# Kernel tuning notes

Measured on AMD Instinct MI355X. Metric: run time of the kernel, lower is better.

The kernel has to match this reference:

```python
import jax, jax.numpy as jnp
import numpy as np


def conv2d(x, w, pad=0, groups=1, bias=None):
    out = jax.lax.conv_general_dilated(
        x, w, (1, 1), [(pad, pad), (pad, pad)],
        dimension_numbers=('NCHW', 'OIHW', 'NCHW'), feature_group_count=groups)
    return out if bias is None else out + bias[None, :, None, None]


def l2norm(t):
    # F.normalize(t, dim=-1): divide by max(||t||_2, 1e-12)
    return t / jnp.maximum(jnp.sqrt(jnp.sum(t * t, axis=-1, keepdims=True)), 1e-12)


def chan_attn(q, k, v, temp, heads):
    # transposed (channel) attention: contract over N=H*W, softmax over small channel dim
    b, _, h, w = v.shape
    n = h * w
    q = l2norm(q.reshape(b, heads, -1, n))
    k = l2norm(k.reshape(b, heads, -1, n))
    v = v.reshape(b, heads, -1, n)
    attn = jax.nn.softmax(jnp.einsum('bhdn,bhen->bhde', q, k) * temp, axis=-1)
    return jnp.einsum('bhde,bhen->bhdn', attn, v).reshape(b, -1, h, w)


def nearest_resize(x, H, W):
    # torch F.interpolate(mode='nearest'): idx = floor(i * in/out)
    hi, wi = x.shape[2], x.shape[3]
    iy = jnp.arange(H) * hi // H
    ix = jnp.arange(W) * wi // W
    return x[:, :, iy][:, :, :, ix]


def deform_conv(x, offsets, w, bias, k, pad, groups):
    # torchvision DeformConv2d, stride=1, dilation=1, offset layout [B, 2*k*k, H, W] as (dy, dx) pairs
    B, Cin, H, W = x.shape
    K2 = k * k
    off = offsets.reshape(B, K2, 2, H, W)
    ky, kx = jnp.meshgrid(jnp.arange(k), jnp.arange(k), indexing='ij')
    py = (jnp.arange(H)[None, None, :, None] - pad) + ky.reshape(1, K2, 1, 1) + off[:, :, 0]
    px = (jnp.arange(W)[None, None, None, :] - pad) + kx.reshape(1, K2, 1, 1) + off[:, :, 1]
    y0f = jnp.floor(py); x0f = jnp.floor(px)
    wy = (py - y0f)[:, None]  # [B,1,K2,H,W]
    wx = (px - x0f)[:, None]
    y0 = y0f.astype(jnp.int32); x0 = x0f.astype(jnp.int32)
    xf = x.reshape(B, Cin, H * W)

    def gather(yi, xi):
        valid = ((yi >= 0) & (yi < H) & (xi >= 0) & (xi < W)).astype(x.dtype)
        idx = (jnp.clip(yi, 0, H - 1) * W + jnp.clip(xi, 0, W - 1)).reshape(B, 1, -1)
        v = jnp.take_along_axis(xf, idx, axis=2).reshape(B, Cin, K2, H, W)
        return v * valid[:, None]

    s = (gather(y0, x0) * (1 - wy) * (1 - wx)
         + gather(y0, x0 + 1) * (1 - wy) * wx
         + gather(y0 + 1, x0) * wy * (1 - wx)
         + gather(y0 + 1, x0 + 1) * wy * wx)  # [B, Cin, K2, H, W]
    g = groups
    s = s.reshape(B, g, Cin // g, K2, H, W)
    wg = w.reshape(g, w.shape[0] // g, Cin // g, K2)
    out = jnp.einsum('bgckhw,gock->bgohw', s, wg).reshape(B, -1, H, W)
    return out + bias[None, :, None, None]


def scconv(x, w_k2, w_k3, w_k4):
    B, C, H, W = x.shape
    p = x.reshape(B, C, H // 2, 2, W // 2, 2).mean(axis=(3, 5))  # AvgPool2d(2,2)
    a = jax.nn.sigmoid(nearest_resize(conv2d(p, w_k2, pad=0), H, W))
    return conv2d(conv2d(x, w_k3, pad=1) * a, w_k4, pad=1)


def layernorm_c(x, g, b):
    # LayerNorm over channel dim of NCHW (applied as [B, HW, C] in the original)
    b_, c, h, w = x.shape
    t = x.reshape(b_, c, h * w).transpose(0, 2, 1)
    mu = t.mean(-1, keepdims=True)
    var = ((t - mu) ** 2).mean(-1, keepdims=True)
    t = (t - mu) / jnp.sqrt(var + 1e-5) * g + b
    return t.transpose(0, 2, 1).reshape(b_, c, h, w)


def _forward(x, y, temp, w_po, w_lp1, w_lp2, ln_g, ln_b, temp_in, w_qkv, w_qkvd,
             w_mproj, w_c3, w_k2, w_k3, w_k4, w_d3, b_d3, w_d5, b_d5, w_d7, b_d7,
             w_pw, b_pw):
    b, c, h, w = x.shape
    heads = 8
    # --- Multi_Receptive_Attentive_Prompts ---
    l1 = conv2d(x, w_lp1)
    l2 = conv2d(x, w_lp2, pad=1)
    xn = layernorm_c(x, ln_g, ln_b)
    qkv = conv2d(conv2d(xn, w_qkv), w_qkvd, pad=1, groups=c)
    qi, ki, vi = jnp.split(qkv, 3, axis=1)
    xg = x + conv2d(chan_attn(qi, ki, vi, temp_in, heads), w_mproj)
    prompt = conv2d(jnp.concatenate([l1, l2, xg], axis=1), w_c3, pad=1)
    # --- Temporal_Alignment ---
    offs = scconv(jnp.concatenate([x, y], axis=1), w_k2, w_k3, w_k4)  # [B,166,H,W]
    f3 = jax.nn.relu(deform_conv(x, offs[:, :18], w_d3, b_d3, 3, 1, 8))
    f5 = jax.nn.relu(deform_conv(x, offs[:, 18:68], w_d5, b_d5, 5, 2, 8))
    f7 = jax.nn.relu(deform_conv(x, offs[:, 68:166], w_d7, b_d7, 7, 3, 8))
    k_feat = conv2d(jnp.concatenate([f3, f5, f7], axis=1), w_pw, bias=b_pw)
    # --- prompted channel attention ---
    q_feat = jnp.concatenate([x, prompt], axis=1)  # 2c channels -> d_q = 2c/heads
    out = chan_attn(q_feat, k_feat, x, temp, heads)  # [B, 2c, H, W]
    return conv2d(out, w_po)


def setup_inputs() -> dict:
    key = jax.random.key(0)
    ks = jax.random.split(key, 16)
    C, B, H, W = 32, 2, 128, 128
    r = lambda k, shp: jax.random.normal(k, shp, dtype=jnp.float32) * 0.05
    return {
        'x': jax.random.normal(ks[0], (B, C, H, W), dtype=jnp.float32),
        'y': jax.random.normal(ks[1], (B, C, H, W), dtype=jnp.float32),
        'temp': jnp.ones((1, 8, 1, 1), jnp.float32),
        'w_po': r(ks[2], (C, 2 * C, 1, 1)),
        'w_lp1': r(ks[3], (C, C, 1, 1)),
        'w_lp2': r(ks[4], (C, C, 3, 3)),
        'ln_g': jnp.ones((C,), jnp.float32),
        'ln_b': jnp.zeros((C,), jnp.float32),
        'temp_in': jnp.ones((1, 8, 1, 1), jnp.float32),
        'w_qkv': r(ks[5], (3 * C, C, 1, 1)),
        'w_qkvd': r(ks[6], (3 * C, 3, 3, 3)),  # groups=C: in/groups = 3
        'w_mproj': r(ks[7], (C, C, 1, 1)),
        'w_c3': r(ks[8], (C, 3 * C, 3, 3)),
        'w_k2': r(ks[9], (166, 2 * C, 3, 3)),
        'w_k3': r(ks[10], (166, 2 * C, 3, 3)),
        'w_k4': r(ks[11], (166, 166, 3, 3)),
        'w_d3': r(ks[12], (C, C // 8, 3, 3)),
        'b_d3': jnp.zeros((C,), jnp.float32),
        'w_d5': r(ks[13], (C, C // 8, 5, 5)),
        'b_d5': jnp.zeros((C,), jnp.float32),
        'w_d7': r(ks[14], (C, C // 8, 7, 7)),
        'b_d7': jnp.zeros((C,), jnp.float32),
        'w_pw': r(ks[15], (C, 3 * C, 1, 1)),
        'b_pw': jnp.zeros((C,), jnp.float32),
    }


def reference(x, y, temp, w_po, w_lp1, w_lp2, ln_g, ln_b, temp_in, w_qkv, w_qkvd,
              w_mproj, w_c3, w_k2, w_k3, w_k4, w_d3, b_d3, w_d5, b_d5, w_d7, b_d7,
              w_pw, b_pw):
    return _forward(x, y, temp, w_po, w_lp1, w_lp2, ln_g, ln_b, temp_in, w_qkv,
                    w_qkvd, w_mproj, w_c3, w_k2, w_k3, w_k4, w_d3, b_d3, w_d5,
                    b_d5, w_d7, b_d7, w_pw, b_pw)
```

## Files before the change

### kernel.cpp

```cpp
#include <hip/hip_runtime.h>
#include <hip/hip_bf16.h>
#include <hip/hip_fp16.h>


constexpr int B = 2, C = 32, H = 128, W = 128, N = H * W;

using bh8   = __attribute__((ext_vector_type(8))) short;
using f32x4 = __attribute__((ext_vector_type(4))) float;

__device__ __forceinline__ ushort f2bf(float v) {
  __hip_bfloat16 h = __float2bfloat16(v);
  return *(ushort*)&h;
}
__device__ __forceinline__ float bf2f(ushort u) {
  union { unsigned int i; float f; } w; w.i = ((unsigned int)u) << 16; return w.f;
}

__global__ __launch_bounds__(256) void k_prep(const float* __restrict__ x,
                                              const float* __restrict__ y,
                                              const float* __restrict__ ln_g,
                                              const float* __restrict__ ln_b,
                                              float* __restrict__ cat2,
                                              ushort* __restrict__ xtb,
                                              ushort* __restrict__ cat2b,
                                              ushort* __restrict__ xnb,
                                              ushort* __restrict__ poolb) {
  __shared__ float tile[C][257];
  const int b = blockIdx.y, n0 = blockIdx.x * 256, tid = threadIdx.x;
  const int n = n0 + tid;
  const int prow = blockIdx.x;
  for (int c = 0; c < C; c++) {
    float v = x[(size_t)(b * C + c) * N + n];
    tile[c][tid] = v;
    cat2[(size_t)(b * 64 + c) * N + n] = v;
  }
  __syncthreads();
  {
    float s = 0.f, ss = 0.f;
#pragma unroll
    for (int c = 0; c < C; c++) { const float v = tile[c][tid]; s += v; ss += v * v; }
    const float mu = s * (1.f / C);
    const float var = ss * (1.f / C) - mu * mu;
    const float inv = rsqrtf(var + 1e-5f);
    ushort xo[32];
#pragma unroll
    for (int c = 0; c < C; c++)
      xo[c] = f2bf((tile[c][tid] - mu) * inv * ln_g[c] + ln_b[c]);
    ushort* dp = xnb + ((size_t)b * N + n) * 32;
#pragma unroll
    for (int k = 0; k < 4; k++) *(bh8*)(dp + k * 8) = *(const bh8*)&xo[k * 8];
  }
  for (int i = tid; i < C * 256; i += 256) {
    int c = i & 31, nl = i >> 5;
    const ushort bv = f2bf(tile[c][nl]);
    xtb[((size_t)b * N + n0 + nl) * 32 + c] = bv;
    cat2b[((size_t)b * N + n0 + nl) * 64 + c] = bv;
  }
  for (int i = tid; i < 2048; i += 256) {
    const int ox = i >> 5, c = i & 31;
    const float pv = 0.25f * (tile[c][2 * ox] + tile[c][2 * ox + 1]
                            + tile[c][128 + 2 * ox] + tile[c][128 + 2 * ox + 1]);
    poolb[((size_t)b * 4096 + prow * 64 + ox) * 64 + c] = f2bf(pv);
  }
  __syncthreads();
  for (int c = 0; c < C; c++) {
    float v = y[(size_t)(b * C + c) * N + n];
    tile[c][tid] = v;
    cat2[(size_t)(b * 64 + 32 + c) * N + n] = v;
  }
  __syncthreads();
  for (int i = tid; i < C * 256; i += 256) {
    int c = i & 31, nl = i >> 5;
    cat2b[((size_t)b * N + n0 + nl) * 64 + 32 + c] = f2bf(tile[c][nl]);
  }
  for (int i = tid; i < 2048; i += 256) {
    const int ox = i >> 5, c = i & 31;
    const float pv = 0.25f * (tile[c][2 * ox] + tile[c][2 * ox + 1]
                            + tile[c][128 + 2 * ox] + tile[c][128 + 2 * ox + 1]);
    poolb[((size_t)b * 4096 + prow * 64 + ox) * 64 + 32 + c] = f2bf(pv);
  }
}

struct WEnt { const float* src; ushort* dst; int cout_real, cin_real, kc32, total; };
struct WArgs { WEnt e[5]; };

__global__ __launch_bounds__(256) void k_wpack(WArgs a) {
  const WEnt en = a.e[blockIdx.y];
  const int tk = 9 * en.kc32;
  for (int i = blockIdx.x * 256 + threadIdx.x; i < en.total; i += gridDim.x * 256) {
    const int co = i / tk, rem = i - co * tk;
    const int t = rem / en.kc32, ci = rem - t * en.kc32;
    float v = 0.f;
    if (co < en.cout_real && ci < en.cin_real)
      v = en.src[((size_t)co * en.cin_real + ci) * 9 + t];
    en.dst[i] = f2bf(v);
  }
}

__global__ __launch_bounds__(256)
void k_castw(const float* __restrict__ a, ushort* __restrict__ da, int na,
             const float* __restrict__ b2, ushort* __restrict__ db, int nb2) {
  const int i = blockIdx.x * 256 + threadIdx.x;
  if (i < na) da[i] = f2bf(a[i]);
  if (i < nb2) db[i] = f2bf(b2[i]);
}

template <int MT, int KC>
__global__ __launch_bounds__(256)
void k_gemm1x1(const ushort* __restrict__ in, int in_cs,
               const ushort* __restrict__ wq, const float* __restrict__ bias,
               float* __restrict__ out, long out_bs) {
  const int tid = threadIdx.x, b = blockIdx.y;
  const int px0 = blockIdx.x * 64 + (tid >> 6) * 16;
  const int lane = tid & 63, q = lane >> 4, n = lane & 15, q8 = q * 8;
  f32x4 acc[MT];
#pragma unroll
  for (int mt = 0; mt < MT; mt++) acc[mt] = (f32x4){0.f, 0.f, 0.f, 0.f};
  const ushort* ib = in + (size_t)b * N * in_cs;
#pragma unroll
  for (int kc = 0; kc < KC; kc++) {
    const bh8 bb = *(const bh8*)(ib + (size_t)(px0 + n) * in_cs + kc * 32 + q8);
#pragma unroll
    for (int mt = 0; mt < MT; mt++) {
      const bh8 a = *(const bh8*)(wq + (size_t)(mt * 16 + n) * (KC * 32) + kc * 32 + q8);
      acc[mt] = __builtin_amdgcn_mfma_f32_16x16x32_bf16(a, bb, acc[mt], 0, 0, 0);
    }
  }
  float* ob = out + (size_t)b * out_bs;
#pragma unroll
  for (int mt = 0; mt < MT; mt++)
#pragma unroll
    for (int r = 0; r < 4; r++) {
      const int co = mt * 16 + q * 4 + r;
      const float bv = bias ? bias[co] : 0.f;
      ob[(size_t)co * N + px0 + n] = acc[mt][r] + bv;
    }
}

__global__ __launch_bounds__(256)
void k_conv3m(const ushort* __restrict__ xin, long in_bs, int in_cs, int ih, int iw,
              const ushort* __restrict__ wp, int kchunks, int cout_real,
              void* __restrict__ outp, long out_bs, int out_coff,
              int oh, int ow, int pad, int omode, int out_cs, int store_tot,
              const float* __restrict__ gatep) {
  __shared__ ushort smem[17408];
  ushort* xt = smem;
  const int tid = threadIdx.x, b = blockIdx.z;
  const int y0 = blockIdx.x * 2, co0 = blockIdx.y * 32;
  const int wv = tid >> 6, lane = tid & 63;
  const int row_sel = wv >> 1, col0 = (wv & 1) * 64;
  const int q = lane >> 4, n = lane & 15, q8 = q * 8;
  const int kc32 = kchunks * 32;
  const ushort* xb = xin + (size_t)b * in_bs;

  f32x4 acc[2][4];
#pragma unroll
  for (int mt = 0; mt < 2; mt++)
#pragma unroll
    for (int nb = 0; nb < 4; nb++) acc[mt][nb] = (f32x4){0.f, 0.f, 0.f, 0.f};

  for (int cc = 0; cc < kchunks; cc++) {
    __syncthreads();
    for (int i = tid; i < 2080; i += 256) {
      const int qq = i & 3, rc = i >> 2;
      const int r = rc / 130, c = rc - r * 130;
      const int yy = y0 - pad + r, xx = c - pad;
      bh8 v = {0, 0, 0, 0, 0, 0, 0, 0};
      if (yy >= 0 && yy < ih && xx >= 0 && xx < iw)
        v = *(const bh8*)(xb + ((size_t)yy * iw + xx) * in_cs + cc * 32 + qq * 8);
      *(bh8*)&xt[rc * 32 + qq * 8] = v;
    }
    __syncthreads();
#pragma unroll
    for (int t = 0; t < 9; t++) {
      const int dy = t / 3, dx = t - dy * 3;
      bh8 a[2], bb[4];
#pragma unroll
      for (int mt = 0; mt < 2; mt++)
        a[mt] = *(const bh8*)(wp + (size_t)((co0 + mt * 16 + n) * 9 + t) * kc32 + cc * 32 + q8);
#pragma unroll
      for (int nb = 0; nb < 4; nb++)
        bb[nb] = *(const bh8*)&xt[((row_sel + dy) * 130 + col0 + nb * 16 + n + dx) * 32 + q8];
#pragma unroll
      for (int mt = 0; mt < 2; mt++)
#pragma unroll
        for (int nb = 0; nb < 4; nb++)
          acc[mt][nb] = __builtin_amdgcn_mfma_f32_16x16x32_bf16(a[mt], bb[nb], acc[mt][nb], 0, 0, 0);
    }
  }

  const size_t osp = (size_t)oh * ow;
  if (omode == 0) {
    const int oy = y0 + row_sel;
    float* ob = (float*)outp + (size_t)b * out_bs + (size_t)out_coff * osp + (size_t)oy * ow;
#pragma unroll
    for (int mt = 0; mt < 2; mt++)
#pragma unroll
      for (int r = 0; r < 4; r++) {
        const int co = co0 + mt * 16 + q * 4 + r;
        if (co < cout_real) {
#pragma unroll
          for (int nb = 0; nb < 4; nb++) {
            const int px = col0 + nb * 16 + n;
            if (px < ow) ob[(size_t)co * osp + px] = acc[mt][nb][r];
          }
        }
      }
  } else if (omode == 1) {
    __syncthreads();
#pragma unroll
    for (int mt = 0; mt < 2; mt++)
#pragma unroll
      for (int nb = 0; nb < 4; nb++) {
        const int px = col0 + nb * 16 + n;
        ushort4 o;
        o.x = f2bf(acc[mt][nb][0]); o.y = f2bf(acc[mt][nb][1]);
        o.z = f2bf(acc[mt][nb][2]); o.w = f2bf(acc[mt][nb][3]);
        *(ushort4*)&smem[(row_sel * 128 + px) * 36 + mt * 16 + q * 4] = o;
      }
    __syncthreads();
    {
      const int row = tid >> 7, px = tid & 127;
      const int oy2 = y0 + row;
      const int sc = min(32, store_tot - co0);
      if (px < ow && sc > 0) {
        ushort* dst = (ushort*)outp + ((size_t)b * osp + (size_t)oy2 * ow + px) * out_cs
                      + out_coff + co0;
        const ushort* src = &smem[(row * 128 + px) * 36];
        if (gatep) {
          const int iy = (oy2 * 62) >> 7, ix2 = (px * 62) >> 7;
          const float* gp = gatep + ((size_t)b * 3844 + iy * 62 + ix2) * 168;
          for (int c = 0; c < sc; c += 4) {
            ushort4 v = *(const ushort4*)(src + c);
            const int ch0 = out_coff + co0 + c;
            float g0 = 1.f, g1 = 1.f, g2 = 1.f, g3 = 1.f;
            if (ch0 + 3 < 166) {
              const float4 a4 = *(const float4*)(gp + ch0);
              g0 = 1.f / (1.f + expf(-a4.x)); g1 = 1.f / (1.f + expf(-a4.y));
              g2 = 1.f / (1.f + expf(-a4.z)); g3 = 1.f / (1.f + expf(-a4.w));
            } else {
              if (ch0 + 0 < 166) g0 = 1.f / (1.f + expf(-gp[ch0 + 0]));
              if (ch0 + 1 < 166) g1 = 1.f / (1.f + expf(-gp[ch0 + 1]));
              if (ch0 + 2 < 166) g2 = 1.f / (1.f + expf(-gp[ch0 + 2]));
              if (ch0 + 3 < 166) g3 = 1.f / (1.f + expf(-gp[ch0 + 3]));
            }
            v.x = f2bf(bf2f(v.x) * g0); v.y = f2bf(bf2f(v.y) * g1);
            v.z = f2bf(bf2f(v.z) * g2); v.w = f2bf(bf2f(v.w) * g3);
            *(ushort4*)(dst + c) = v;
          }
        } else {
          for (int c = 0; c < sc; c += 4)
            *(ushort4*)(dst + c) = *(const ushort4*)(src + c);
        }
      }
    }
  } else {
    float* tf = (float*)smem;
    for (int round = 0; round < 2; round++) {
      __syncthreads();
      if (row_sel == round) {
#pragma unroll
        for (int mt = 0; mt < 2; mt++)
#pragma unroll
          for (int nb = 0; nb < 4; nb++) {
            const int px = col0 + nb * 16 + n;
            *(f32x4*)&tf[px * 34 + mt * 16 + q * 4] = acc[mt][nb];
          }
      }
      __syncthreads();
      const int px = tid & 127, half = tid >> 7;
      const int oy2 = y0 + round;
      if (px < ow) {
        float* dst = (float*)outp + ((size_t)b * osp + (size_t)oy2 * ow + px) * out_cs
                     + out_coff + co0 + half * 16;
        const float* src = &tf[px * 34 + half * 16];
        for (int c = 0; c < 16; c += 4) {
          if (co0 + half * 16 + c + 3 < store_tot)
            *(float4*)(dst + c) = *(const float4*)(src + c);
        }
      }
    }
  }
}

template <int PX>
__global__ __launch_bounds__(256)
void k_conv1x1v(const float* __restrict__ in, long in_bs, int cin,
                const float* __restrict__ wts, const float* __restrict__ bias,
                float* __restrict__ out, long out_bs, int out_coff,
                ushort* __restrict__ outb, int ob_cs) {
  const int n0 = (blockIdx.x * 256 + threadIdx.x) * PX;
  const int co0 = blockIdx.y * 4, b = blockIdx.z;
  const float* ip = in + (size_t)b * in_bs + n0;
  const float* w = wts + (size_t)co0 * cin;
  float acc[4][PX] = {};
  for (int ci = 0; ci < cin; ci++) {
    float xv[PX];
    if (PX == 4) {
      const float4 v = *(const float4*)(ip + (size_t)ci * N);
      xv[0] = v.x; xv[1] = v.y; xv[2] = v.z; xv[3] = v.w;
    } else {
      const float2 v = *(const float2*)(ip + (size_t)ci * N);
      xv[0] = v.x; xv[1] = v.y;
    }
    const float w0 = w[ci], w1 = w[cin + ci], w2 = w[2 * cin + ci], w3 = w[3 * cin + ci];
#pragma unroll
    for (int p = 0; p < PX; p++) {
      acc[0][p] += xv[p] * w0; acc[1][p] += xv[p] * w1;
      acc[2][p] += xv[p] * w2; acc[3][p] += xv[p] * w3;
    }
  }
  if (bias) {
#pragma unroll
    for (int o = 0; o < 4; o++) {
      const float bv = bias[co0 + o];
#pragma unroll
      for (int p = 0; p < PX; p++) acc[o][p] += bv;
    }
  }
  if (outb) {
#pragma unroll
    for (int p = 0; p < PX; p++) {
      ushort4 o;
      o.x = f2bf(acc[0][p]); o.y = f2bf(acc[1][p]);
      o.z = f2bf(acc[2][p]); o.w = f2bf(acc[3][p]);
      *(ushort4*)(outb + ((size_t)b * N + n0 + p) * ob_cs + out_coff + co0) = o;
    }
  } else {
#pragma unroll
    for (int o = 0; o < 4; o++) {
      if (PX == 4)
        *(float4*)(out + (size_t)b * out_bs + (size_t)(out_coff + co0 + o) * N + n0) =
            make_float4(acc[o][0], acc[o][1], acc[o][2], acc[o][3]);
      else
        *(float2*)(out + (size_t)b * out_bs + (size_t)(out_coff + co0 + o) * N + n0) =
            make_float2(acc[o][0], acc[o][1]);
    }
  }
}

__global__ __launch_bounds__(256) void k_dwconv(const float* __restrict__ in,
                                                const float* __restrict__ wts,
                                                float* __restrict__ out) {
  const int n0 = (blockIdx.x * 256 + threadIdx.x) * 4;
  const int g = blockIdx.y, b = blockIdx.z;
  const int h0 = n0 >> 7, w0 = n0 & 127;
  float acc[3][4] = {};
  for (int ci = 0; ci < 3; ci++) {
    const float* ip = in + ((size_t)b * 96 + g * 3 + ci) * N;
    float v[3][6];
#pragma unroll
    for (int r = 0; r < 3; r++) {
      const int iy = h0 - 1 + r;
      const bool rowok = (iy >= 0) & (iy < H);
#pragma unroll
      for (int j = 0; j < 6; j++) {
        const int ix = w0 - 1 + j;
        v[r][j] = (rowok && ix >= 0 && ix < W) ? ip[(size_t)iy * W + ix] : 0.f;
      }
    }
#pragma unroll
    for (int o = 0; o < 3; o++) {
      const float* wp = wts + ((size_t)(g * 3 + o) * 3 + ci) * 9;
#pragma unroll
      for (int r = 0; r < 3; r++) {
        const float wa = wp[r * 3 + 0], wb = wp[r * 3 + 1], wc = wp[r * 3 + 2];
#pragma unroll
        for (int p = 0; p < 4; p++)
          acc[o][p] += v[r][p] * wa + v[r][p + 1] * wb + v[r][p + 2] * wc;
      }
    }
  }
#pragma unroll
  for (int o = 0; o < 3; o++)
    *(float4*)(out + ((size_t)b * 96 + g * 3 + o) * N + n0) =
        make_float4(acc[o][0], acc[o][1], acc[o][2], acc[o][3]);
}

template <int DQ>
__global__ __launch_bounds__(256)
void k_attn_part(const float* __restrict__ q1, long q1_bs,
                 const float* __restrict__ q2, long q2_bs,
                 const float* __restrict__ k, long k_bs,
                 float* __restrict__ partial) {
  const int h = blockIdx.x, b = blockIdx.y, ch = blockIdx.z, tid = threadIdx.x;
  const float* qp[DQ];
#pragma unroll
  for (int d = 0; d < DQ; d++) {
    const int qc = h * DQ + d;
    qp[d] = (qc < 32) ? (q1 + (size_t)b * q1_bs + (size_t)qc * N)
                      : (q2 + (size_t)b * q2_bs + (size_t)(qc - 32) * N);
  }
  const float* kp[4];
#pragma unroll
  for (int e = 0; e < 4; e++) kp[e] = k + (size_t)b * k_bs + (size_t)(h * 4 + e) * N;

  constexpr int NV = DQ + 4 + DQ * 4;
  float ssq[DQ] = {}, ssk[4] = {}, gr[DQ][4] = {};
  const int n1 = (ch + 1) * (N / 16);
  for (int n = ch * (N / 16) + tid; n < n1; n += 256) {
    float qv[DQ], kv[4];
#pragma unroll
    for (int d = 0; d < DQ; d++) { qv[d] = qp[d][n]; ssq[d] += qv[d] * qv[d]; }
#pragma unroll
    for (int e = 0; e < 4; e++) { kv[e] = kp[e][n]; ssk[e] += kv[e] * kv[e]; }
#pragma unroll
    for (int d = 0; d < DQ; d++)
#pragma unroll
      for (int e = 0; e < 4; e++) gr[d][e] += qv[d] * kv[e];
  }
  float vals[NV];
#pragma unroll
  for (int d = 0; d < DQ; d++) vals[d] = ssq[d];
#pragma unroll
  for (int e = 0; e < 4; e++) vals[DQ + e] = ssk[e];
#pragma unroll
  for (int d = 0; d < DQ; d++)
#pragma unroll
    for (int e = 0; e < 4; e++) vals[DQ + 4 + d * 4 + e] = gr[d][e];
#pragma unroll
  for (int j = 0; j < NV; j++) {
    float v = vals[j];
    for (int m = 32; m > 0; m >>= 1) v += __shfl_xor(v, m, 64);
    vals[j] = v;
  }
  __shared__ float red[4][NV];
  const int wid = tid >> 6, lane = tid & 63;
  if (lane == 0)
#pragma unroll
    for (int j = 0; j < NV; j++) red[wid][j] = vals[j];
  __syncthreads();
  if (tid < NV)
    partial[(size_t)(((b * 8 + h) * 16) + ch) * NV + tid] =
        red[0][tid] + red[1][tid] + red[2][tid] + red[3][tid];
}

template <int DQ>
__global__ __launch_bounds__(128)
void k_attn_soft(const float* __restrict__ partial,
                 const float* __restrict__ temp, float* __restrict__ stats) {
  constexpr int NV = DQ + 4 + DQ * 4;
  const int h = blockIdx.x, b = blockIdx.y, tid = threadIdx.x;
  __shared__ float tot[NV];
  if (tid < NV) {
    float s = 0.f;
#pragma unroll
    for (int ch = 0; ch < 16; ch++)
      s += partial[(size_t)(((b * 8 + h) * 16) + ch) * NV + tid];
    tot[tid] = s;
  }
  __syncthreads();
  if (tid == 0) {
    float invq[DQ], invk[4];
#pragma unroll
    for (int d = 0; d < DQ; d++) invq[d] = 1.f / fmaxf(sqrtf(tot[d]), 1e-12f);
#pragma unroll
    for (int e = 0; e < 4; e++) invk[e] = 1.f / fmaxf(sqrtf(tot[DQ + e]), 1e-12f);
    const float t = temp[h];
    float* sp = stats + (size_t)(b * 8 + h) * DQ * 4;
    for (int d = 0; d < DQ; d++) {
      float s[4], mx = -1e30f;
#pragma unroll
      for (int e = 0; e < 4; e++) {
        s[e] = tot[DQ + 4 + d * 4 + e] * invq[d] * invk[e] * t;
        mx = fmaxf(mx, s[e]);
      }
      float sum = 0.f;
#pragma unroll
      for (int e = 0; e < 4; e++) { s[e] = expf(s[e] - mx); sum += s[e]; }
#pragma unroll
      for (int e = 0; e < 4; e++) sp[d * 4 + e] = s[e] / sum;
    }
  }
}

template <int DQ>
__global__ __launch_bounds__(256)
void k_fold(const float* __restrict__ stats, const float* __restrict__ w,
            float* __restrict__ M) {
  const int b = blockIdx.x;
  for (int idx = threadIdx.x; idx < 1024; idx += 256) {
    const int co = idx >> 5, j = idx & 31;
    const int h = j >> 2, e = j & 3;
    const float* A = stats + ((size_t)b * 8 + h) * DQ * 4;
    const float* wr = w + co * (8 * DQ) + h * DQ;
    float s = 0.f;
#pragma unroll
    for (int d = 0; d < DQ; d++) s += wr[d] * A[d * 4 + e];
    M[((size_t)b * 32 + co) * 32 + j] = s;
  }
}

__global__ __launch_bounds__(256)
void k_attn_mproj2(const float* __restrict__ qkv2, const float* __restrict__ M2,
                   const float* __restrict__ x, ushort* __restrict__ cat1b) {
  __shared__ float mls[512];
  const int tid = threadIdx.x, b = blockIdx.y, z = blockIdx.z;
  const int n = blockIdx.x * 256 + tid;
  for (int i = tid; i < 512; i += 256)
    mls[i] = M2[((size_t)b * 32 + z * 16) * 32 + i];
  __syncthreads();
  const float* vi = qkv2 + (size_t)b * (96L * N) + 64L * N;
  float vv[32];
#pragma unroll
  for (int ci = 0; ci < 32; ci++) vv[ci] = vi[(size_t)ci * N + n];
  ushort to[16];
  for (int o = 0; o < 16; o++) {
    const float* m = &mls[o * 32];
    float r = 0.f;
#pragma unroll
    for (int ci = 0; ci < 32; ci += 4) {
      const float4 w4 = *(const float4*)&m[ci];
      r += w4.x * vv[ci] + w4.y * vv[ci + 1] + w4.z * vv[ci + 2] + w4.w * vv[ci + 3];
    }
    r += x[(size_t)(b * 64 + z * 16 + o) * N + n];
    to[o] = f2bf(r);
  }
  ushort* dp = cat1b + ((size_t)b * N + n) * 96 + 64 + z * 16;
#pragma unroll
  for (int k = 0; k < 2; k++) *(bh8*)(dp + k * 8) = *(const bh8*)&to[k * 8];
}

__global__ __launch_bounds__(256)
void k_attn_po2(const float* __restrict__ cat2, const float* __restrict__ M,
                float* __restrict__ outp) {
  __shared__ float mls[512];
  const int tid = threadIdx.x, b = blockIdx.y, z = blockIdx.z;
  const int n = blockIdx.x * 256 + tid;
  for (int i = tid; i < 512; i += 256)
    mls[i] = M[((size_t)b * 32 + z * 16) * 32 + i];
  __syncthreads();
  const float* v = cat2 + (size_t)b * (64L * N);
  float vv[32];
#pragma unroll
  for (int ci = 0; ci < 32; ci++) vv[ci] = v[(size_t)ci * N + n];
  for (int o = 0; o < 16; o++) {
    const float* m = &mls[o * 32];
    float r = 0.f;
#pragma unroll
    for (int ci = 0; ci < 32; ci += 4) {
      const float4 w4 = *(const float4*)&m[ci];
      r += w4.x * vv[ci] + w4.y * vv[ci + 1] + w4.z * vv[ci + 2] + w4.w * vv[ci + 3];
    }
    outp[(size_t)(b * 32 + z * 16 + o) * N + n] = r;
  }
}

__global__ __launch_bounds__(256)
void k_deform7(const ushort* __restrict__ xtb, const float* __restrict__ offs,
               const float* __restrict__ wd3, const float* __restrict__ bd3,
               const float* __restrict__ wd5, const float* __restrict__ bd5,
               const float* __restrict__ wd7, const float* __restrict__ bd7,
               ushort* __restrict__ cat3b) {
  const int tid = threadIdx.x, b = blockIdx.y;
  const int zone = blockIdx.x >> 9;
  const int blk = blockIdx.x & 511;
  int K, off_c0, out_c0;
  const float *wd, *bd;
  if (zone == 0)      { K = 3; off_c0 = 0;  out_c0 = 0;  wd = wd3; bd = bd3; }
  else if (zone == 1) { K = 5; off_c0 = 18; out_c0 = 32; wd = wd5; bd = bd5; }
  else                { K = 7; off_c0 = 68; out_c0 = 64; wd = wd7; bd = bd7; }
  const int K2 = K * K, PAD = K / 2;

  extern __shared__ __align__(16) char smem[];
  __half*  wlds = (__half*)smem;
  __half*  wbl  = wlds + K2 * 128;
  ushort*  abl  = (ushort*)(wbl + 32 * K2 * 4);

  for (int i = tid; i < K2 * 128; i += 256) {
    const int t = i >> 7, r = i & 127;
    const int g = r >> 4, oo = (r >> 2) & 3, ci = r & 3;
    wlds[i] = __float2half(wd[(size_t)((g * 4 + oo) * 4 + ci) * K2 + t]);
  }
  const int px0 = blk * 32;
  const float* obb = offs + ((size_t)b * N) * 168;
  for (int i = tid; i < 32 * K2; i += 256) {
    const int p = i / K2, t = i - p * K2;
    const int px = px0 + p;
    const int hy = px >> 7, wx = px & 127;
    const int ky = t / K, kx = t - ky * K;
    const float* ob2 = obb + (size_t)px * 168 + off_c0;
    const float dy = ob2[2 * t];
    const float dx = ob2[2 * t + 1];
    const float py = (float)(hy - PAD + ky) + dy;
    const float pxf = (float)(wx - PAD + kx) + dx;
    const float y0f = floorf(py), x0f = floorf(pxf);
    const float fy = py - y0f, fx = pxf - x0f;
    const int y0 = (int)y0f, x0 = (int)x0f;
    const int y1 = y0 + 1, x1 = x0 + 1;
    float w00 = (1.f - fy) * (1.f - fx), w01 = (1.f - fy) * fx;
    float w10 = fy * (1.f - fx), w11 = fy * fx;
    const bool vy0 = (y0 >= 0) & (y0 < H), vy1 = (y1 >= 0) & (y1 < H);
    const bool vx0 = (x0 >= 0) & (x0 < W), vx1 = (x1 >= 0) & (x1 < W);
    w00 = (vy0 & vx0) ? w00 : 0.f;
    w01 = (vy0 & vx1) ? w01 : 0.f;
    w10 = (vy1 & vx0) ? w10 : 0.f;
    w11 = (vy1 & vx1) ? w11 : 0.f;
    const int cy0 = min(max(y0, 0), H - 1), cy1 = min(max(y1, 0), H - 1);
    const int cx0 = min(max(x0, 0), W - 1), cx1 = min(max(x1, 0), W - 1);
    const int base = (p * K2 + t) * 4;
    wbl[base + 0] = __float2half(w00); wbl[base + 1] = __float2half(w01);
    wbl[base + 2] = __float2half(w10); wbl[base + 3] = __float2half(w11);
    abl[base + 0] = (ushort)(cy0 * W + cx0);
    abl[base + 1] = (ushort)(cy0 * W + cx1);
    abl[base + 2] = (ushort)(cy1 * W + cx0);
    abl[base + 3] = (ushort)(cy1 * W + cx1);
  }
  __syncthreads();

  const int pxl = tid >> 3, g = tid & 7;
  const int px = px0 + pxl;
  const ushort* xb = xtb + (size_t)b * N * 32 + g * 4;
  float acc[4] = {0.f, 0.f, 0.f, 0.f};
  for (int t = 0; t < K2; t++) {
    const int base = (pxl * K2 + t) * 4;
    const ushort4 r4 = *(const ushort4*)&abl[base];
    const float2 w01v = __half22float2(*(const __half2*)&wbl[base]);
    const float2 w23v = __half22float2(*(const __half2*)&wbl[base + 2]);
    const ushort4 c0 = *(const ushort4*)(xb + (size_t)r4.x * 32);
    const ushort4 c1 = *(const ushort4*)(xb + (size_t)r4.y * 32);
    const ushort4 c2 = *(const ushort4*)(xb + (size_t)r4.z * 32);
    const ushort4 c3 = *(const ushort4*)(xb + (size_t)r4.w * 32);
    const float s0 = w01v.x * bf2f(c0.x) + w01v.y * bf2f(c1.x)
                   + w23v.x * bf2f(c2.x) + w23v.y * bf2f(c3.x);
    const float s1 = w01v.x * bf2f(c0.y) + w01v.y * bf2f(c1.y)
                   + w23v.x * bf2f(c2.y) + w23v.y * bf2f(c3.y);
    const float s2 = w01v.x * bf2f(c0.z) + w01v.y * bf2f(c1.z)
                   + w23v.x * bf2f(c2.z) + w23v.y * bf2f(c3.z);
    const float s3 = w01v.x * bf2f(c0.w) + w01v.y * bf2f(c1.w)
                   + w23v.x * bf2f(c2.w) + w23v.y * bf2f(c3.w);
    const __half2* wp2 = (const __half2*)&wlds[(t * 8 + g) * 16];
#pragma unroll
    for (int oo = 0; oo < 4; oo++) {
      const float2 u01 = __half22float2(wp2[oo * 2]);
      const float2 u23 = __half22float2(wp2[oo * 2 + 1]);
      acc[oo] += s0 * u01.x + s1 * u01.y + s2 * u23.x + s3 * u23.y;
    }
  }
  ushort4 o;
  o.x = f2bf(fmaxf(acc[0] + bd[g * 4 + 0], 0.f));
  o.y = f2bf(fmaxf(acc[1] + bd[g * 4 + 1], 0.f));
  o.z = f2bf(fmaxf(acc[2] + bd[g * 4 + 2], 0.f));
  o.w = f2bf(fmaxf(acc[3] + bd[g * 4 + 3], 0.f));
  *(ushort4*)(cat3b + ((size_t)b * N + px) * 96 + out_c0 + g * 4) = o;
}

extern "C" void kernel_launch(void* const* d_in, const int* in_sizes, int n_in,
                              void* d_out, int out_size, void* d_ws, size_t ws_size,
                              hipStream_t stream) {
  const float* fx       = (const float*)d_in[0];
  const float* fy       = (const float*)d_in[1];
  const float* w_temp   = (const float*)d_in[2];
  const float* w_po     = (const float*)d_in[3];
  const float* w_lp1    = (const float*)d_in[4];
  const float* w_lp2    = (const float*)d_in[5];
  const float* ln_g     = (const float*)d_in[6];
  const float* ln_b     = (const float*)d_in[7];
  const float* w_tempin = (const float*)d_in[8];
  const float* w_qkv    = (const float*)d_in[9];
  const float* w_qkvd   = (const float*)d_in[10];
  const float* w_mproj  = (const float*)d_in[11];
  const float* w_c3     = (const float*)d_in[12];
  const float* w_k2     = (const float*)d_in[13];
  const float* w_k3     = (const float*)d_in[14];
  const float* w_k4     = (const float*)d_in[15];
  const float* w_d3     = (const float*)d_in[16];
  const float* b_d3     = (const float*)d_in[17];
  const float* w_d5     = (const float*)d_in[18];
  const float* b_d5     = (const float*)d_in[19];
  const float* w_d7     = (const float*)d_in[20];
  const float* b_d7     = (const float*)d_in[21];
  const float* w_pw     = (const float*)d_in[22];
  const float* b_pw     = (const float*)d_in[23];
  float* ws = (float*)d_ws;

  size_t off = 0;
  auto buf = [&](size_t nelem) { float* p = ws + off; off += nelem; return p; };
  float* CAT2   = buf(2097152);
  float* XTBf   = buf(1048576);
  float* R1     = buf(1048576);
  float* R2     = buf(3145728);
  float* R3     = buf(3145728);
  float* PROMPT = buf(1048576);
  float* R4     = buf(5439488);
  float* OFFS   = buf(5505024);
  float* STATS  = buf(65536);
  float* CAT2Bf = buf(524288);
  float* WPf    = buf(327680);
  float* POOLBf = buf(262144);
  (void)ws_size; (void)out_size; (void)n_in; (void)in_sizes;

  float* QKV1 = R2;
  float* QKV2 = R3;   float* ASMALL = R3 + 524288;
  float* KFEAT = R4 + 3145728;
  float* ST_IN = STATS;
  float* ST_FI = STATS + 256;
  float* M_IN  = STATS + 1024;
  float* M_FI  = STATS + 3072;
  float* P_IN  = STATS + 5120;
  float* P_FI  = STATS + 14336;

  ushort* XTb   = (ushort*)XTBf;
  ushort* XNb   = (ushort*)R1;
  ushort* CAT2b = (ushort*)CAT2Bf;
  ushort* POOLb = (ushort*)POOLBf;
  ushort* CAT1b = (ushort*)OFFS;
  ushort* CAT3b = (ushort*)R4;
  ushort* T3b   = (ushort*)R2;

  ushort* WPu = (ushort*)WPf;
  ushort* wp_lp2 = WPu;
  ushort* wp_c3  = wp_lp2 + 18432;
  ushort* wp_k2  = wp_c3 + 55296;
  ushort* wp_k3  = wp_k2 + 110592;
  ushort* wp_k4  = wp_k3 + 110592;
  ushort* wq_qkv = wp_k4 + 331776;
  ushort* wq_pw  = wq_qkv + 3072;

  const long bs64 = 64L * N, bs32 = 32L * N, bs96 = 96L * N;

  WArgs wa;
  wa.e[0] = { w_lp2, wp_lp2, 32, 32, 32, 64 * 9 * 32 };
  wa.e[1] = { w_c3,  wp_c3,  32, 96, 96, 64 * 9 * 96 };
  wa.e[2] = { w_k2,  wp_k2, 166, 64, 64, 192 * 9 * 64 };
  wa.e[3] = { w_k3,  wp_k3, 166, 64, 64, 192 * 9 * 64 };
  wa.e[4] = { w_k4,  wp_k4, 166, 166, 192, 192 * 9 * 192 };
  k_wpack<<<dim3(64, 5), 256, 0, stream>>>(wa);
  k_castw<<<dim3(12), 256, 0, stream>>>(w_qkv, wq_qkv, 3072, w_pw, wq_pw, 3072);
  k_prep<<<dim3(N / 256, B), 256, 0, stream>>>(
      fx, fy, ln_g, ln_b, CAT2, XTb, CAT2b, XNb, POOLb);
  k_gemm1x1<6, 1><<<dim3(N / 64, B), 256, 0, stream>>>(
      XNb, 32, wq_qkv, nullptr, QKV1, bs96);
  k_dwconv<<<dim3(N / 1024, 32, B), 256, 0, stream>>>(QKV1, w_qkvd, QKV2);
  k_attn_part<4><<<dim3(8, B, 16), 256, 0, stream>>>(
      QKV2, bs96, nullptr, 0, QKV2 + bs32, bs96, P_IN);
  k_attn_soft<4><<<dim3(8, B), 128, 0, stream>>>(P_IN, w_tempin, ST_IN);
  k_fold<4><<<dim3(B), 256, 0, stream>>>(ST_IN, w_mproj, M_IN);
  k_attn_mproj2<<<dim3(N / 256, B, 2), 256, 0, stream>>>(QKV2, M_IN, CAT2, CAT1b);
  k_conv1x1v<2><<<dim3(N / 512, 8, B), 256, 0, stream>>>(
      CAT2, bs64, 32, w_lp1, nullptr, nullptr, 0, 0, CAT1b, 96);
  k_conv3m<<<dim3(64, 1, B), 256, 0, stream>>>(
      CAT2b, (long)N * 64, 64, H, W, wp_lp2, 1, 32, CAT1b, 0, 32, H, W, 1, 1, 96, 32,
      nullptr);
  k_conv3m<<<dim3(64, 1, B), 256, 0, stream>>>(
      CAT1b, (long)N * 96, 96, H, W, wp_c3, 3, 32, PROMPT, bs32, 0, H, W, 1, 0, 0, 0,
      nullptr);
  k_conv3m<<<dim3(31, 6, B), 256, 0, stream>>>(
      POOLb, 4096L * 64, 64, 64, 64, wp_k2, 2, 166, ASMALL, 0, 0, 62, 62, 0, 2, 168, 168,
      nullptr);
  k_conv3m<<<dim3(64, 6, B), 256, 0, stream>>>(
      CAT2b, (long)N * 64, 64, H, W, wp_k3, 2, 166, T3b, 0, 0, H, W, 1, 1, 192, 192,
      ASMALL);
  k_conv3m<<<dim3(64, 6, B), 256, 0, stream>>>(
      T3b, (long)N * 192, 192, H, W, wp_k4, 6, 166, OFFS, 0, 0, H, W, 1, 2, 168, 168,
      nullptr);
  {
    const int K2m = 49;
    const size_t smem = (size_t)K2m * 128 * 2 + (size_t)32 * K2m * 4 * 2 * 2;
    k_deform7<<<dim3(3 * (N / 32), B), 256, smem, stream>>>(
        XTb, OFFS, w_d3, b_d3, w_d5, b_d5, w_d7, b_d7, CAT3b);
  }
  k_gemm1x1<2, 3><<<dim3(N / 64, B), 256, 0, stream>>>(
      CAT3b, 96, wq_pw, b_pw, KFEAT, bs32);
  k_attn_part<8><<<dim3(8, B, 16), 256, 0, stream>>>(
      CAT2, bs64, PROMPT, bs32, KFEAT, bs32, P_FI);
  k_attn_soft<8><<<dim3(8, B), 128, 0, stream>>>(P_FI, w_temp, ST_FI);
  k_fold<8><<<dim3(B), 256, 0, stream>>>(ST_FI, w_po, M_FI);
  k_attn_po2<<<dim3(N / 256, B, 2), 256, 0, stream>>>(CAT2, M_FI, (float*)d_out);
}
```

Measured before the change: 409.1 us.

## Fuse softmax with fold, merge lp1 into mproj kernel, drop fp32 y copy

Merges the attention softmax and weight-fold steps into one kernel, folds the 1x1 lp1 convolution into the mproj kernel as a second z-slice, and moves the qkv/pw weight casts into the weight-pack kernel. The prep kernel no longer writes an fp32 copy of y; only x is kept in a 32-channel fp32 buffer. The aim is fewer kernel launches and less redundant global memory traffic, at the cost of slightly more per-block work in the fused kernels.

```diff
diff --git a/kernel.cpp b/kernel.cpp
--- a/kernel.cpp
+++ b/kernel.cpp
@@ -20,7 +20,7 @@
                                               const float* __restrict__ y,
                                               const float* __restrict__ ln_g,
                                               const float* __restrict__ ln_b,
-                                              float* __restrict__ cat2,
+                                              float* __restrict__ x32,
                                               ushort* __restrict__ xtb,
                                               ushort* __restrict__ cat2b,
                                               ushort* __restrict__ xnb,
@@ -32,7 +32,7 @@
   for (int c = 0; c < C; c++) {
     float v = x[(size_t)(b * C + c) * N + n];
     tile[c][tid] = v;
-    cat2[(size_t)(b * 64 + c) * N + n] = v;
+    x32[(size_t)(b * 32 + c) * N + n] = v;
   }
   __syncthreads();
   {
@@ -63,11 +63,8 @@
     poolb[((size_t)b * 4096 + prow * 64 + ox) * 64 + c] = f2bf(pv);
   }
   __syncthreads();
-  for (int c = 0; c < C; c++) {
-    float v = y[(size_t)(b * C + c) * N + n];
-    tile[c][tid] = v;
-    cat2[(size_t)(b * 64 + 32 + c) * N + n] = v;
-  }
+  for (int c = 0; c < C; c++)
+    tile[c][tid] = y[(size_t)(b * C + c) * N + n];
   __syncthreads();
   for (int i = tid; i < C * 256; i += 256) {
     int c = i & 31, nl = i >> 5;
@@ -82,10 +79,15 @@
 }
 
 struct WEnt { const float* src; ushort* dst; int cout_real, cin_real, kc32, total; };
-struct WArgs { WEnt e[5]; };
+struct WArgs { WEnt e[7]; };
 
 __global__ __launch_bounds__(256) void k_wpack(WArgs a) {
   const WEnt en = a.e[blockIdx.y];
+  if (en.kc32 == 0) {
+    for (int i = blockIdx.x * 256 + threadIdx.x; i < en.total; i += gridDim.x * 256)
+      en.dst[i] = f2bf(en.src[i]);
+    return;
+  }
   const int tk = 9 * en.kc32;
   for (int i = blockIdx.x * 256 + threadIdx.x; i < en.total; i += gridDim.x * 256) {
     const int co = i / tk, rem = i - co * tk;
@@ -95,14 +97,6 @@
       v = en.src[((size_t)co * en.cin_real + ci) * 9 + t];
     en.dst[i] = f2bf(v);
   }
-}
-
-__global__ __launch_bounds__(256)
-void k_castw(const float* __restrict__ a, ushort* __restrict__ da, int na,
-             const float* __restrict__ b2, ushort* __restrict__ db, int nb2) {
-  const int i = blockIdx.x * 256 + threadIdx.x;
-  if (i < na) da[i] = f2bf(a[i]);
-  if (i < nb2) db[i] = f2bf(b2[i]);
 }
 
 template <int MT, int KC>
@@ -283,62 +277,6 @@
   }
 }
 
-template <int PX>
-__global__ __launch_bounds__(256)
-void k_conv1x1v(const float* __restrict__ in, long in_bs, int cin,
-                const float* __restrict__ wts, const float* __restrict__ bias,
-                float* __restrict__ out, long out_bs, int out_coff,
-                ushort* __restrict__ outb, int ob_cs) {
-  const int n0 = (blockIdx.x * 256 + threadIdx.x) * PX;
-  const int co0 = blockIdx.y * 4, b = blockIdx.z;
-  const float* ip = in + (size_t)b * in_bs + n0;
-  const float* w = wts + (size_t)co0 * cin;
-  float acc[4][PX] = {};
-  for (int ci = 0; ci < cin; ci++) {
-    float xv[PX];
-    if (PX == 4) {
-      const float4 v = *(const float4*)(ip + (size_t)ci * N);
-      xv[0] = v.x; xv[1] = v.y; xv[2] = v.z; xv[3] = v.w;
-    } else {
-      const float2 v = *(const float2*)(ip + (size_t)ci * N);
-      xv[0] = v.x; xv[1] = v.y;
-    }
-    const float w0 = w[ci], w1 = w[cin + ci], w2 = w[2 * cin + ci], w3 = w[3 * cin + ci];
-#pragma unroll
-    for (int p = 0; p < PX; p++) {
-      acc[0][p] += xv[p] * w0; acc[1][p] += xv[p] * w1;
-      acc[2][p] += xv[p] * w2; acc[3][p] += xv[p] * w3;
-    }
-  }
-  if (bias) {
-#pragma unroll
-    for (int o = 0; o < 4; o++) {
-      const float bv = bias[co0 + o];
-#pragma unroll
-      for (int p = 0; p < PX; p++) acc[o][p] += bv;
-    }
-  }
-  if (outb) {
-#pragma unroll
-    for (int p = 0; p < PX; p++) {
-      ushort4 o;
-      o.x = f2bf(acc[0][p]); o.y = f2bf(acc[1][p]);
-      o.z = f2bf(acc[2][p]); o.w = f2bf(acc[3][p]);
-      *(ushort4*)(outb + ((size_t)b * N + n0 + p) * ob_cs + out_coff + co0) = o;
-    }
-  } else {
-#pragma unroll
-    for (int o = 0; o < 4; o++) {
-      if (PX == 4)
-        *(float4*)(out + (size_t)b * out_bs + (size_t)(out_coff + co0 + o) * N + n0) =
-            make_float4(acc[o][0], acc[o][1], acc[o][2], acc[o][3]);
-      else
-        *(float2*)(out + (size_t)b * out_bs + (size_t)(out_coff + co0 + o) * N + n0) =
-            make_float2(acc[o][0], acc[o][1]);
-    }
-  }
-}
-
 __global__ __launch_bounds__(256) void k_dwconv(const float* __restrict__ in,
                                                 const float* __restrict__ wts,
                                                 float* __restrict__ out) {
@@ -437,11 +375,12 @@
 
 template <int DQ>
 __global__ __launch_bounds__(128)
-void k_attn_soft(const float* __restrict__ partial,
-                 const float* __restrict__ temp, float* __restrict__ stats) {
+void k_softfold(const float* __restrict__ partial, const float* __restrict__ temp,
+                const float* __restrict__ w, float* __restrict__ M) {
   constexpr int NV = DQ + 4 + DQ * 4;
   const int h = blockIdx.x, b = blockIdx.y, tid = threadIdx.x;
   __shared__ float tot[NV];
+  __shared__ float als[DQ * 4];
   if (tid < NV) {
     float s = 0.f;
 #pragma unroll
@@ -457,7 +396,6 @@
 #pragma unroll
     for (int e = 0; e < 4; e++) invk[e] = 1.f / fmaxf(sqrtf(tot[DQ + e]), 1e-12f);
     const float t = temp[h];
-    float* sp = stats + (size_t)(b * 8 + h) * DQ * 4;
     for (int d = 0; d < DQ; d++) {
       float s[4], mx = -1e30f;
 #pragma unroll
@@ -469,43 +407,39 @@
 #pragma unroll
       for (int e = 0; e < 4; e++) { s[e] = expf(s[e] - mx); sum += s[e]; }
 #pragma unroll
-      for (int e = 0; e < 4; e++) sp[d * 4 + e] = s[e] / sum;
-    }
-  }
-}
-
-template <int DQ>
+      for (int e = 0; e < 4; e++) als[d * 4 + e] = s[e] / sum;
+    }
+  }
+  __syncthreads();
+  const int co = tid >> 2, e = tid & 3;
+  const float* wr = w + co * (8 * DQ) + h * DQ;
+  float s = 0.f;
+#pragma unroll
+  for (int d = 0; d < DQ; d++) s += wr[d] * als[d * 4 + e];
+  M[((size_t)b * 32 + co) * 32 + h * 4 + e] = s;
+}
+
 __global__ __launch_bounds__(256)
-void k_fold(const float* __restrict__ stats, const float* __restrict__ w,
-            float* __restrict__ M) {
-  const int b = blockIdx.x;
-  for (int idx = threadIdx.x; idx < 1024; idx += 256) {
-    const int co = idx >> 5, j = idx & 31;
-    const int h = j >> 2, e = j & 3;
-    const float* A = stats + ((size_t)b * 8 + h) * DQ * 4;
-    const float* wr = w + co * (8 * DQ) + h * DQ;
-    float s = 0.f;
-#pragma unroll
-    for (int d = 0; d < DQ; d++) s += wr[d] * A[d * 4 + e];
-    M[((size_t)b * 32 + co) * 32 + j] = s;
-  }
-}
-
-__global__ __launch_bounds__(256)
-void k_attn_mproj2(const float* __restrict__ qkv2, const float* __restrict__ M2,
-                   const float* __restrict__ x, ushort* __restrict__ cat1b) {
-  __shared__ float mls[512];
+void k_mproj_lp1(const float* __restrict__ qkv2, const float* __restrict__ M2,
+                 const float* __restrict__ w_lp1, const float* __restrict__ x32,
+                 ushort* __restrict__ cat1b) {
+  __shared__ float mls[1024];
   const int tid = threadIdx.x, b = blockIdx.y, z = blockIdx.z;
   const int n = blockIdx.x * 256 + tid;
-  for (int i = tid; i < 512; i += 256)
-    mls[i] = M2[((size_t)b * 32 + z * 16) * 32 + i];
-  __syncthreads();
-  const float* vi = qkv2 + (size_t)b * (96L * N) + 64L * N;
+  const float* msrc = (z == 0) ? w_lp1 : (M2 + (size_t)b * 1024);
+  for (int i = tid; i < 1024; i += 256) mls[i] = msrc[i];
+  __syncthreads();
   float vv[32];
-#pragma unroll
-  for (int ci = 0; ci < 32; ci++) vv[ci] = vi[(size_t)ci * N + n];
-  ushort to[16];
-  for (int o = 0; o < 16; o++) {
+  if (z == 0) {
+#pragma unroll
+    for (int ci = 0; ci < 32; ci++) vv[ci] = x32[(size_t)(b * 32 + ci) * N + n];
+  } else {
+    const float* vi = qkv2 + (size_t)b * (96L * N) + 64L * N;
+#pragma unroll
+    for (int ci = 0; ci < 32; ci++) vv[ci] = vi[(size_t)ci * N + n];
+  }
+  ushort to[32];
+  for (int o = 0; o < 32; o++) {
     const float* m = &mls[o * 32];
     float r = 0.f;
 #pragma unroll
@@ -513,16 +447,16 @@
       const float4 w4 = *(const float4*)&m[ci];
       r += w4.x * vv[ci] + w4.y * vv[ci + 1] + w4.z * vv[ci + 2] + w4.w * vv[ci + 3];
     }
-    r += x[(size_t)(b * 64 + z * 16 + o) * N + n];
+    if (z == 1) r += x32[(size_t)(b * 32 + o) * N + n];
     to[o] = f2bf(r);
   }
-  ushort* dp = cat1b + ((size_t)b * N + n) * 96 + 64 + z * 16;
-#pragma unroll
-  for (int k = 0; k < 2; k++) *(bh8*)(dp + k * 8) = *(const bh8*)&to[k * 8];
+  ushort* dp = cat1b + ((size_t)b * N + n) * 96 + (z ? 64 : 0);
+#pragma unroll
+  for (int k = 0; k < 4; k++) *(bh8*)(dp + k * 8) = *(const bh8*)&to[k * 8];
 }
 
 __global__ __launch_bounds__(256)
-void k_attn_po2(const float* __restrict__ cat2, const float* __restrict__ M,
+void k_attn_po2(const float* __restrict__ x32, const float* __restrict__ M,
                 float* __restrict__ outp) {
   __shared__ float mls[512];
   const int tid = threadIdx.x, b = blockIdx.y, z = blockIdx.z;
@@ -530,7 +464,7 @@
   for (int i = tid; i < 512; i += 256)
     mls[i] = M[((size_t)b * 32 + z * 16) * 32 + i];
   __syncthreads();
-  const float* v = cat2 + (size_t)b * (64L * N);
+  const float* v = x32 + (size_t)b * (32L * N);
   float vv[32];
 #pragma unroll
   for (int ci = 0; ci < 32; ci++) vv[ci] = v[(size_t)ci * N + n];
@@ -676,7 +610,7 @@
 
   size_t off = 0;
   auto buf = [&](size_t nelem) { float* p = ws + off; off += nelem; return p; };
-  float* CAT2   = buf(2097152);
+  float* X32    = buf(1048576);
   float* XTBf   = buf(1048576);
   float* R1     = buf(1048576);
   float* R2     = buf(3145728);
@@ -693,8 +627,6 @@
   float* QKV1 = R2;
   float* QKV2 = R3;   float* ASMALL = R3 + 524288;
   float* KFEAT = R4 + 3145728;
-  float* ST_IN = STATS;
-  float* ST_FI = STATS + 256;
   float* M_IN  = STATS + 1024;
   float* M_FI  = STATS + 3072;
   float* P_IN  = STATS + 5120;
@@ -717,7 +649,7 @@
   ushort* wq_qkv = wp_k4 + 331776;
   ushort* wq_pw  = wq_qkv + 3072;
 
-  const long bs64 = 64L * N, bs32 = 32L * N, bs96 = 96L * N;
+  const long bs32 = 32L * N, bs96 = 96L * N;
 
   WArgs wa;
   wa.e[0] = { w_lp2, wp_lp2, 32, 32, 32, 64 * 9 * 32 };
@@ -725,20 +657,18 @@
   wa.e[2] = { w_k2,  wp_k2, 166, 64, 64, 192 * 9 * 64 };
   wa.e[3] = { w_k3,  wp_k3, 166, 64, 64, 192 * 9 * 64 };
   wa.e[4] = { w_k4,  wp_k4, 166, 166, 192, 192 * 9 * 192 };
-  k_wpack<<<dim3(64, 5), 256, 0, stream>>>(wa);
-  k_castw<<<dim3(12), 256, 0, stream>>>(w_qkv, wq_qkv, 3072, w_pw, wq_pw, 3072);
+  wa.e[5] = { w_qkv, wq_qkv, 0, 0, 0, 3072 };
+  wa.e[6] = { w_pw,  wq_pw,  0, 0, 0, 3072 };
+  k_wpack<<<dim3(64, 7), 256, 0, stream>>>(wa);
   k_prep<<<dim3(N / 256, B), 256, 0, stream>>>(
-      fx, fy, ln_g, ln_b, CAT2, XTb, CAT2b, XNb, POOLb);
+      fx, fy, ln_g, ln_b, X32, XTb, CAT2b, XNb, POOLb);
   k_gemm1x1<6, 1><<<dim3(N / 64, B), 256, 0, stream>>>(
       XNb, 32, wq_qkv, nullptr, QKV1, bs96);
   k_dwconv<<<dim3(N / 1024, 32, B), 256, 0, stream>>>(QKV1, w_qkvd, QKV2);
   k_attn_part<4><<<dim3(8, B, 16), 256, 0, stream>>>(
       QKV2, bs96, nullptr, 0, QKV2 + bs32, bs96, P_IN);
-  k_attn_soft<4><<<dim3(8, B), 128, 0, stream>>>(P_IN, w_tempin, ST_IN);
-  k_fold<4><<<dim3(B), 256, 0, stream>>>(ST_IN, w_mproj, M_IN);
-  k_attn_mproj2<<<dim3(N / 256, B, 2), 256, 0, stream>>>(QKV2, M_IN, CAT2, CAT1b);
-  k_conv1x1v<2><<<dim3(N / 512, 8, B), 256, 0, stream>>>(
-      CAT2, bs64, 32, w_lp1, nullptr, nullptr, 0, 0, CAT1b, 96);
+  k_softfold<4><<<dim3(8, B), 128, 0, stream>>>(P_IN, w_tempin, w_mproj, M_IN);
+  k_mproj_lp1<<<dim3(N / 256, B, 2), 256, 0, stream>>>(QKV2, M_IN, w_lp1, X32, CAT1b);
   k_conv3m<<<dim3(64, 1, B), 256, 0, stream>>>(
       CAT2b, (long)N * 64, 64, H, W, wp_lp2, 1, 32, CAT1b, 0, 32, H, W, 1, 1, 96, 32,
       nullptr);
@@ -763,8 +693,7 @@
   k_gemm1x1<2, 3><<<dim3(N / 64, B), 256, 0, stream>>>(
       CAT3b, 96, wq_pw, b_pw, KFEAT, bs32);
   k_attn_part<8><<<dim3(8, B, 16), 256, 0, stream>>>(
-      CAT2, bs64, PROMPT, bs32, KFEAT, bs32, P_FI);
-  k_attn_soft<8><<<dim3(8, B), 128, 0, stream>>>(P_FI, w_temp, ST_FI);
-  k_fold<8><<<dim3(B), 256, 0, stream>>>(ST_FI, w_po, M_FI);
-  k_attn_po2<<<dim3(N / 256, B, 2), 256, 0, stream>>>(CAT2, M_FI, (float*)d_out);
-}
+      X32, bs32, PROMPT, bs32, KFEAT, bs32, P_FI);
+  k_softfold<8><<<dim3(8, B), 128, 0, stream>>>(P_FI, w_temp, w_po, M_FI);
+  k_attn_po2<<<dim3(N / 256, B, 2), 256, 0, stream>>>(X32, M_FI, (float*)d_out);
+}
```

Result: faster. 396.3 us (median of 2 runs) (-3.1%).
